# Kernel tuning notes

Hardware: AMD Instinct MI355X
Metric: run time of the kernel (lower is better)

The kernel has to match this reference:

```python
import jax, jax.numpy as jnp
import numpy as np

N_ENT = 200000  # entities per graph (sr and tg)
E = 4_000_000   # triples per graph
R_SR, R_TG, D = 1000, 1200, 128


def _cosine_sim_nbyn(a, b):
    a = a * jax.lax.rsqrt(jnp.sum(a * a, -1, keepdims=True) + 1e-8)
    b = b * jax.lax.rsqrt(jnp.sum(b * b, -1, keepdims=True) + 1e-8)
    return a @ b.T


def _relation_weighting(a, b):
    # pad to square, cosine similarity, max-pool rows/cols (MuGNN RelationWeighting)
    ra, rb = a.shape[0], b.shape[0]
    n = max(ra, rb)
    a_p = jnp.pad(a, ((0, n - ra), (0, 0)))
    b_p = jnp.pad(b, ((0, n - rb), (0, 0)))
    sim = _cosine_sim_nbyn(a_p, b_p)  # [n, n]
    return jnp.max(sim, axis=1)[:ra], jnp.max(sim, axis=0)[:rb]


def _normalize_adj(rows, cols, vals, n):
    # symmetric normalization D^-1/2 A D^-1/2 on COO values
    deg = jax.ops.segment_sum(vals, rows, num_segments=n)
    d_is = jnp.where(deg > 0, jax.lax.rsqrt(jnp.maximum(deg, 1e-12)), 0.0)
    return vals * d_is[rows] * d_is[cols]


def _adjacency_side(head, tail, conf, imp, pca, n):
    # g_func_template: elementwise product of the three aligned sparse matrices
    vals = conf * imp * pca
    # + unit (identity) matrix, then normalize; coords = [edges ; diagonal]
    diag = jnp.arange(n)
    rows = jnp.concatenate([head, diag])
    cols = jnp.concatenate([tail, diag])
    allv = jnp.concatenate([vals, jnp.ones((n,), vals.dtype)])
    return _normalize_adj(rows, cols, allv, n)  # [E+n] COO values


def setup_inputs() -> dict:
    key = jax.random.key(0)
    ks = jax.random.split(key, 14)
    return {
        "rel_emb_sr": jax.random.normal(ks[0], (R_SR, D), jnp.float32),
        "rel_emb_tg": jax.random.normal(ks[1], (R_TG, D), jnp.float32),
        "conf_sr": jax.random.uniform(ks[2], (E,), jnp.float32),
        "imp_sr": jax.random.uniform(ks[3], (E,), jnp.float32),
        "pca_sr": jax.random.uniform(ks[4], (E,), jnp.float32),
        "conf_tg": jax.random.uniform(ks[5], (E,), jnp.float32),
        "imp_tg": jax.random.uniform(ks[6], (E,), jnp.float32),
        "pca_tg": jax.random.uniform(ks[7], (E,), jnp.float32),
        "head_sr": jax.random.randint(ks[8], (E,), 0, N_ENT),
        "tail_sr": jax.random.randint(ks[9], (E,), 0, N_ENT),
        "relation_sr": jax.random.randint(ks[10], (E,), 0, R_SR),
        "head_tg": jax.random.randint(ks[11], (E,), 0, N_ENT),
        "tail_tg": jax.random.randint(ks[12], (E,), 0, N_ENT),
        "relation_tg": jax.random.randint(ks[13], (E,), 0, R_TG),
    }


def reference(rel_emb_sr, rel_emb_tg, conf_sr, imp_sr, pca_sr,
              conf_tg, imp_tg, pca_tg,
              head_sr, tail_sr, relation_sr, head_tg, tail_tg, relation_tg):
    # relation weighting (computed in the original forward; g_func_template
    # discards the gathered relation attention, so relation_sr/tg do not
    # affect the adjacency values)
    rw_sr, rw_tg = _relation_weighting(rel_emb_sr, rel_emb_tg)
    adj_sr = _adjacency_side(head_sr, tail_sr, conf_sr, imp_sr, pca_sr, N_ENT)
    adj_tg = _adjacency_side(head_tg, tail_tg, conf_tg, imp_tg, pca_tg, N_ENT)
    # adjacency returned as normalized COO values on constant coords
    return adj_sr, adj_tg, rw_sr, rw_tg
```

## Files before the change

### kernel.cpp

```cpp
#include <hip/hip_runtime.h>
#include <stdint.h>

#define N_ENT 200000
#define NEDGE 4000000
#define RSR 1000
#define RTG 1200
#define DIM 128

#define NBUCK 196
#define BUCKSZ 1024
#define CAP 22272
#define CHUNK 8192
#define NTA 512
#define NE4 (NEDGE / 4)
#define NBLK 489
#define PER (NEDGE + N_ENT)
#define PER4 (PER / 4)
#define ATILES 16
#define BTILES 19
#define NRW 2240

typedef float f32x4 __attribute__((ext_vector_type(4)));
typedef int   i32x4 __attribute__((ext_vector_type(4)));


__global__ void prep_kernel(const float* __restrict__ emb_sr, const float* __restrict__ emb_tg,
                            float* __restrict__ an, float* __restrict__ bn,
                            unsigned* __restrict__ gcount) {
    int blk = blockIdx.x, t = threadIdx.x;
    const float* src; float* dst; int row;
    if (blk < RSR) { src = emb_sr; dst = an; row = blk; }
    else           { src = emb_tg; dst = bn; row = blk - RSR; }
    float x = src[row * DIM + t];
    __shared__ float sh[DIM];
    sh[t] = x * x;
    __syncthreads();
    for (int off = 64; off > 0; off >>= 1) {
        if (t < off) sh[t] += sh[t + off];
        __syncthreads();
    }
    dst[row * DIM + t] = x * rsqrtf(sh[0] + 1e-8f);
    if (blk == 0)
        for (int i = t; i < 2 * NBUCK; i += DIM) gcount[i] = 0;
}


__global__ __launch_bounds__(NTA) void passA_kernel(
        const float* __restrict__ conf_sr, const float* __restrict__ imp_sr,
        const float* __restrict__ pca_sr,
        const float* __restrict__ conf_tg, const float* __restrict__ imp_tg,
        const float* __restrict__ pca_tg,
        const int* __restrict__ head_sr, const int* __restrict__ head_tg,
        float* __restrict__ out_sr, float* __restrict__ out_tg,
        unsigned* __restrict__ gcount, unsigned* __restrict__ regions) {
    __shared__ unsigned cnt[NBUCK];
    __shared__ unsigned offs[NBUCK];
    __shared__ unsigned gdst[NBUCK];
    __shared__ unsigned ssum[256];
    __shared__ unsigned wtot[4];
    __shared__ unsigned stage[CHUNK];

    const int t = threadIdx.x;
    const int side = (int)blockIdx.x >= NBLK;
    const int blk = side ? blockIdx.x - NBLK : blockIdx.x;
    const f32x4* conf4 = (const f32x4*)(side ? conf_tg : conf_sr);
    const f32x4* imp4  = (const f32x4*)(side ? imp_tg  : imp_sr);
    const f32x4* pca4  = (const f32x4*)(side ? pca_tg  : pca_sr);
    const i32x4* head4 = (const i32x4*)(side ? head_tg : head_sr);
    f32x4*       o4    = (f32x4*)(side ? out_tg : out_sr);

    for (int i = t; i < NBUCK; i += NTA) cnt[i] = 0;
    __syncthreads();

    int bkt[16];
    unsigned rec[16], rnk[16];
#pragma unroll
    for (int i = 0; i < 4; i++) {
        int q = blk * 2048 + t + i * NTA;
        if (q < NE4) {
            f32x4 cf = __builtin_nontemporal_load(conf4 + q);
            f32x4 im = __builtin_nontemporal_load(imp4 + q);
            f32x4 pc = __builtin_nontemporal_load(pca4 + q);
            i32x4 hh = head4[q];
            f32x4 v = cf * im * pc;
            o4[q] = v;
            const int hs[4] = {hh.x, hh.y, hh.z, hh.w};
            const float vs[4] = {v.x, v.y, v.z, v.w};
#pragma unroll
            for (int j = 0; j < 4; j++) {
                int h = hs[j];
                int bb = h >> 10;
                unsigned qv = (unsigned)(vs[j] * 16384.f + 0.5f);
                if (qv > 16383u) qv = 16383u;
                bkt[i * 4 + j] = bb;
                rec[i * 4 + j] = ((unsigned)h << 14) | qv;
                rnk[i * 4 + j] = atomicAdd(&cnt[bb], 1u);
            }
        } else {
#pragma unroll
            for (int j = 0; j < 4; j++) bkt[i * 4 + j] = -1;
        }
    }
    __syncthreads();

    if (t < 256) {
        int lane = t & 63, w = t >> 6;
        unsigned s = (t < NBUCK) ? cnt[t] : 0u;
#pragma unroll
        for (int d = 1; d < 64; d <<= 1) {
            unsigned u = __shfl_up(s, d);
            if (lane >= d) s += u;
        }
        if (lane == 63) wtot[w] = s;
        ssum[t] = s;
    }
    __syncthreads();
    unsigned wb0 = wtot[0];
    unsigned wb1 = wb0 + wtot[1];
    unsigned wb2 = wb1 + wtot[2];
    unsigned total = wb2 + wtot[3];
    if (t < NBUCK) {
        int w = t >> 6;
        unsigned add = (w == 0) ? 0u : (w == 1) ? wb0 : (w == 2) ? wb1 : wb2;
        unsigned ex = ssum[t] + add - cnt[t];
        offs[t] = ex;
        unsigned gb = atomicAdd(&gcount[side * NBUCK + t], cnt[t]);
        gdst[t] = (unsigned)(side * NBUCK + t) * CAP + gb - ex;
    }
    __syncthreads();

#pragma unroll
    for (int i = 0; i < 16; i++)
        if (bkt[i] >= 0) stage[offs[bkt[i]] + rnk[i]] = rec[i];
    __syncthreads();

    for (int i = t; i < (int)total; i += NTA) {
        unsigned r = stage[i];
        unsigned b = r >> 24;
        unsigned d = gdst[b] + i;
        if (d < (unsigned)(side * NBUCK + b + 1) * CAP) regions[d] = r;
    }
}


__global__ __launch_bounds__(256) void passB_kernel(const unsigned* __restrict__ regions,
                                                    const unsigned* __restrict__ gcount,
                                                    float* __restrict__ dis) {
    __shared__ float bins[BUCKSZ / 2];
    int t = threadIdx.x;
    int g = blockIdx.x;
    int sb = g >> 1;
    unsigned half = g & 1;
    for (int i = t; i < BUCKSZ / 2; i += 256) bins[i] = 0.f;
    __syncthreads();
    unsigned n = gcount[sb];
    if (n > CAP) n = CAP;
    const unsigned* rp = regions + (size_t)sb * CAP;
    for (unsigned i = t; i < n; i += 256) {
        unsigned r = rp[i];
        unsigned bin = (r >> 14) & (BUCKSZ - 1);
        if ((bin >> 9) == half)
            atomicAdd(&bins[bin & 511u], (float)(r & 16383u) * (1.f / 16384.f));
    }
    __syncthreads();
    int side = sb >= NBUCK;
    int b = side ? sb - NBUCK : sb;
    int base = b * BUCKSZ + (int)half * 512;
    float* dout = dis + (size_t)side * N_ENT;
    for (int i = t; i < 512; i += 256) {
        int e = base + i;
        if (e < N_ENT) dout[e] = rsqrtf(1.0f + bins[i]);
    }
}


__global__ void deg_init_kernel(float* __restrict__ dis) {
    int i = blockIdx.x * 256 + threadIdx.x;
    if (i < (2 * N_ENT) / 4)
        ((float4*)dis)[i] = make_float4(1.f, 1.f, 1.f, 1.f);
}

__global__ void scatter_atomic_kernel(
        const float* __restrict__ conf_sr, const float* __restrict__ imp_sr,
        const float* __restrict__ pca_sr,
        const float* __restrict__ conf_tg, const float* __restrict__ imp_tg,
        const float* __restrict__ pca_tg,
        const int* __restrict__ head_sr, const int* __restrict__ head_tg,
        float* __restrict__ out_sr, float* __restrict__ out_tg,
        float* __restrict__ deg) {
    int e = blockIdx.x * blockDim.x + threadIdx.x;
    if (e < NEDGE) {
        float v = conf_sr[e] * imp_sr[e] * pca_sr[e];
        out_sr[e] = v;
        unsafeAtomicAdd(&deg[head_sr[e]], v);
    } else if (e < 2 * NEDGE) {
        int i = e - NEDGE;
        float v = conf_tg[i] * imp_tg[i] * pca_tg[i];
        out_tg[i] = v;
        unsafeAtomicAdd(&deg[N_ENT + head_tg[i]], v);
    }
}

__global__ void rsqrt_kernel(float* __restrict__ dis) {
    int i = blockIdx.x * blockDim.x + threadIdx.x;
    if (i < 2 * N_ENT) dis[i] = rsqrtf(dis[i]);
}


__global__ __launch_bounds__(256) void finalize_kernel(
        const int* __restrict__ head_sr, const int* __restrict__ tail_sr,
        const int* __restrict__ head_tg, const int* __restrict__ tail_tg,
        const float* __restrict__ dis, float* __restrict__ out,
        const float* __restrict__ rowpart, const float* __restrict__ colpart,
        float* __restrict__ rw_sr, float* __restrict__ rw_tg) {
    int idx = blockIdx.x * blockDim.x + threadIdx.x;
    if (idx >= 2 * PER4) {
        int rid = idx - 2 * PER4;
        if (rid < 1024) {
            if (rid < RSR) {
                float m = -1e30f;
                for (int b = 0; b < BTILES; b++) m = fmaxf(m, rowpart[b * 1024 + rid]);
                rw_sr[rid] = m;
            }
        } else if (rid < NRW) {
            int j = rid - 1024;
            if (j < RTG) {
                float m = -1e30f;
                for (int a = 0; a < ATILES; a++) m = fmaxf(m, colpart[a * 1216 + j]);
                rw_tg[j] = fmaxf(m, 0.0f);
            }
        }
        return;
    }
    int side = idx >= PER4 ? 1 : 0;
    int q = side ? idx - PER4 : idx;
    const float* dg = dis + (size_t)side * N_ENT;
    f32x4* o = (f32x4*)(out + (size_t)side * PER);
    if (q < NE4) {
        const i32x4* hd = (const i32x4*)(side ? head_tg : head_sr);
        const i32x4* tl = (const i32x4*)(side ? tail_tg : tail_sr);
        i32x4 hh = hd[q];
        i32x4 tt = tl[q];
        f32x4 v = o[q];
        v.x *= dg[hh.x] * dg[tt.x];
        v.y *= dg[hh.y] * dg[tt.y];
        v.z *= dg[hh.z] * dg[tt.z];
        v.w *= dg[hh.w] * dg[tt.w];
        o[q] = v;
    } else {
        f32x4 d = ((const f32x4*)dg)[q - NE4];
        o[q] = d * d;
    }
}


__global__ __launch_bounds__(256) void pools_tiles_kernel(
        const float* __restrict__ an, const float* __restrict__ bn,
        float* __restrict__ rowpart, float* __restrict__ colpart) {
    __shared__ float sA[64][132];
    __shared__ float sB[64][133];
    __shared__ float rr[64][17];
    __shared__ float cc[64][17];
    int t = threadIdx.x;
    int atile = blockIdx.x % ATILES;
    int btile = blockIdx.x / ATILES;
    for (int idx = t; idx < 64 * 32; idx += 256) {
        int row = idx >> 5, k4 = idx & 31;
        int ga = atile * 64 + row;
        float4 va = (ga < RSR) ? ((const float4*)(an + ga * DIM))[k4]
                               : make_float4(0.f, 0.f, 0.f, 0.f);
        *(float4*)&sA[row][k4 * 4] = va;
        int gb = btile * 64 + row;
        float4 vb = (gb < RTG) ? ((const float4*)(bn + gb * DIM))[k4]
                               : make_float4(0.f, 0.f, 0.f, 0.f);
        sB[row][k4 * 4 + 0] = vb.x; sB[row][k4 * 4 + 1] = vb.y;
        sB[row][k4 * 4 + 2] = vb.z; sB[row][k4 * 4 + 3] = vb.w;
    }
    __syncthreads();
    int tx = t & 15, ty = t >> 4;
    float acc[4][4] = {};
    for (int k4 = 0; k4 < 32; k4++) {
        float4 a4[4];
#pragma unroll
        for (int r = 0; r < 4; r++) a4[r] = *(const float4*)&sA[ty * 4 + r][k4 * 4];
#pragma unroll
        for (int kk = 0; kk < 4; kk++) {
            float bv[4];
#pragma unroll
            for (int c = 0; c < 4; c++) bv[c] = sB[tx * 4 + c][k4 * 4 + kk];
            float av[4];
#pragma unroll
            for (int r = 0; r < 4; r++)
                av[r] = kk == 0 ? a4[r].x : kk == 1 ? a4[r].y : kk == 2 ? a4[r].z : a4[r].w;
#pragma unroll
            for (int r = 0; r < 4; r++)
#pragma unroll
                for (int c = 0; c < 4; c++) acc[r][c] = fmaf(av[r], bv[c], acc[r][c]);
        }
    }
    float rm[4] = {-1e30f, -1e30f, -1e30f, -1e30f};
    float cm[4] = {-1e30f, -1e30f, -1e30f, -1e30f};
#pragma unroll
    for (int r = 0; r < 4; r++)
#pragma unroll
        for (int c = 0; c < 4; c++) {
            bool jok = (btile * 64 + tx * 4 + c) < RTG;
            rm[r] = fmaxf(rm[r], jok ? acc[r][c] : -1e30f);
            cm[c] = fmaxf(cm[c], acc[r][c]);
        }
#pragma unroll
    for (int r = 0; r < 4; r++) rr[ty * 4 + r][tx] = rm[r];
#pragma unroll
    for (int c = 0; c < 4; c++) cc[tx * 4 + c][ty] = cm[c];
    __syncthreads();
    if (t < 64) {
        float m = rr[t][0];
        for (int x = 1; x < 16; x++) m = fmaxf(m, rr[t][x]);
        rowpart[btile * 1024 + atile * 64 + t] = m;
        float m2 = cc[t][0];
        for (int x = 1; x < 16; x++) m2 = fmaxf(m2, cc[t][x]);
        colpart[atile * 1216 + btile * 64 + t] = m2;
    }
}


extern "C" void kernel_launch(void* const* d_in, const int* in_sizes, int n_in,
                              void* d_out, int out_size, void* d_ws, size_t ws_size,
                              hipStream_t stream) {
    const float* rel_emb_sr = (const float*)d_in[0];
    const float* rel_emb_tg = (const float*)d_in[1];
    const float* conf_sr = (const float*)d_in[2];
    const float* imp_sr  = (const float*)d_in[3];
    const float* pca_sr  = (const float*)d_in[4];
    const float* conf_tg = (const float*)d_in[5];
    const float* imp_tg  = (const float*)d_in[6];
    const float* pca_tg  = (const float*)d_in[7];
    const int* head_sr = (const int*)d_in[8];
    const int* tail_sr = (const int*)d_in[9];
    const int* head_tg = (const int*)d_in[11];
    const int* tail_tg = (const int*)d_in[12];

    float* out = (float*)d_out;
    float* out_sr = out;
    float* out_tg = out + PER;
    float* rw_sr  = out + 2 * (size_t)PER;
    float* rw_tg  = rw_sr + RSR;

    float* ws = (float*)d_ws;
    float* an  = ws;
    float* bn  = an + RSR * DIM;
    float* dis = bn + RTG * DIM;
    unsigned* gcount  = (unsigned*)(dis + 2 * N_ENT);
    unsigned* regions = gcount + 512;
    float* rowpart = (float*)(regions + (size_t)2 * NBUCK * CAP);
    float* colpart = rowpart + BTILES * 1024;

    size_t need = ((size_t)(RSR * DIM + RTG * DIM + 2 * N_ENT + 512) +
                   (size_t)2 * NBUCK * CAP + BTILES * 1024 + ATILES * 1216) * 4;
    bool bucketed = ws_size >= need;

    hipLaunchKernelGGL(prep_kernel, dim3(RSR + RTG), dim3(DIM), 0, stream,
                       rel_emb_sr, rel_emb_tg, an, bn, gcount);

    if (bucketed) {
        hipLaunchKernelGGL(passA_kernel, dim3(2 * NBLK), dim3(NTA), 0, stream,
                           conf_sr, imp_sr, pca_sr, conf_tg, imp_tg, pca_tg,
                           head_sr, head_tg, out_sr, out_tg, gcount, regions);
        hipLaunchKernelGGL(passB_kernel, dim3(4 * NBUCK), dim3(256), 0, stream,
                           regions, gcount, dis);
    } else {
        hipLaunchKernelGGL(deg_init_kernel, dim3((2 * N_ENT / 4 + 255) / 256), dim3(256),
                           0, stream, dis);
        hipLaunchKernelGGL(scatter_atomic_kernel, dim3((2 * NEDGE + 255) / 256), dim3(256),
                           0, stream,
                           conf_sr, imp_sr, pca_sr, conf_tg, imp_tg, pca_tg,
                           head_sr, head_tg, out_sr, out_tg, dis);
        hipLaunchKernelGGL(rsqrt_kernel, dim3((2 * N_ENT + 255) / 256), dim3(256), 0, stream,
                           dis);
    }

    hipLaunchKernelGGL(pools_tiles_kernel, dim3(ATILES * BTILES), dim3(256), 0, stream,
                       an, bn, rowpart, colpart);

    hipLaunchKernelGGL(finalize_kernel, dim3((2 * PER4 + NRW + 255) / 256), dim3(256),
                       0, stream,
                       head_sr, tail_sr, head_tg, tail_tg, dis, out,
                       rowpart, colpart, rw_sr, rw_tg);
}
```

Baseline: 358.0 us.

## Fuse relation-weighting stages into bucketed degree passes to cut kernel launches

Folds the embedding normalization into the first bucketing pass as extra blocks, and the cosine-similarity tile pooling into the second (degree histogram) pass. A memset replaces the counter zeroing, so five launches become a memset plus three kernels. Independent small work can then overlap with the bandwidth-bound edge passes. The finalize kernel also handles both graphs per thread, halving its grid. The risk is heavier kernels with larger shared memory (the fused k2 holds tile buffers), which could lower occupancy for the histogram blocks.

```diff
diff --git a/kernel.cpp b/kernel.cpp
--- a/kernel.cpp
+++ b/kernel.cpp
@@ -14,6 +14,8 @@
 #define NTA 512
 #define NE4 (NEDGE / 4)
 #define NBLK 489
+#define NPREP 550
+#define NPOOLS 304
 #define PER (NEDGE + N_ENT)
 #define PER4 (PER / 4)
 #define ATILES 16
@@ -24,28 +26,9 @@
 typedef int   i32x4 __attribute__((ext_vector_type(4)));
 
 
-__global__ void prep_kernel(const float* __restrict__ emb_sr, const float* __restrict__ emb_tg,
-                            float* __restrict__ an, float* __restrict__ bn,
-                            unsigned* __restrict__ gcount) {
-    int blk = blockIdx.x, t = threadIdx.x;
-    const float* src; float* dst; int row;
-    if (blk < RSR) { src = emb_sr; dst = an; row = blk; }
-    else           { src = emb_tg; dst = bn; row = blk - RSR; }
-    float x = src[row * DIM + t];
-    __shared__ float sh[DIM];
-    sh[t] = x * x;
-    __syncthreads();
-    for (int off = 64; off > 0; off >>= 1) {
-        if (t < off) sh[t] += sh[t + off];
-        __syncthreads();
-    }
-    dst[row * DIM + t] = x * rsqrtf(sh[0] + 1e-8f);
-    if (blk == 0)
-        for (int i = t; i < 2 * NBUCK; i += DIM) gcount[i] = 0;
-}
-
-
-__global__ __launch_bounds__(NTA) void passA_kernel(
+__global__ __launch_bounds__(NTA) void k1_kernel(
+        const float* __restrict__ emb_sr, const float* __restrict__ emb_tg,
+        float* __restrict__ an, float* __restrict__ bn,
         const float* __restrict__ conf_sr, const float* __restrict__ imp_sr,
         const float* __restrict__ pca_sr,
         const float* __restrict__ conf_tg, const float* __restrict__ imp_tg,
@@ -53,6 +36,26 @@
         const int* __restrict__ head_sr, const int* __restrict__ head_tg,
         float* __restrict__ out_sr, float* __restrict__ out_tg,
         unsigned* __restrict__ gcount, unsigned* __restrict__ regions) {
+    const int t = threadIdx.x;
+
+    if (blockIdx.x < NPREP) {
+        __shared__ float sh[NTA];
+        int row = (int)blockIdx.x * 4 + (t >> 7);
+        int col = t & 127;
+        const float* src; float* dst;
+        if (row < RSR) { src = emb_sr + row * DIM; dst = an + row * DIM; }
+        else           { src = emb_tg + (row - RSR) * DIM; dst = bn + (row - RSR) * DIM; }
+        float x = src[col];
+        sh[t] = x * x;
+        __syncthreads();
+        for (int off = 64; off > 0; off >>= 1) {
+            if ((t & 127) < off) sh[t] += sh[t + off];
+            __syncthreads();
+        }
+        dst[col] = x * rsqrtf(sh[(t >> 7) << 7] + 1e-8f);
+        return;
+    }
+
     __shared__ unsigned cnt[NBUCK];
     __shared__ unsigned offs[NBUCK];
     __shared__ unsigned gdst[NBUCK];
@@ -60,9 +63,9 @@
     __shared__ unsigned wtot[4];
     __shared__ unsigned stage[CHUNK];
 
-    const int t = threadIdx.x;
-    const int side = (int)blockIdx.x >= NBLK;
-    const int blk = side ? blockIdx.x - NBLK : blockIdx.x;
+    const int abid = (int)blockIdx.x - NPREP;
+    const int side = abid >= NBLK;
+    const int blk = side ? abid - NBLK : abid;
     const f32x4* conf4 = (const f32x4*)(side ? conf_tg : conf_sr);
     const f32x4* imp4  = (const f32x4*)(side ? imp_tg  : imp_sr);
     const f32x4* pca4  = (const f32x4*)(side ? pca_tg  : pca_sr);
@@ -143,12 +146,87 @@
 }
 
 
-__global__ __launch_bounds__(256) void passB_kernel(const unsigned* __restrict__ regions,
-                                                    const unsigned* __restrict__ gcount,
-                                                    float* __restrict__ dis) {
+__global__ __launch_bounds__(256) void k2_kernel(
+        const float* __restrict__ an, const float* __restrict__ bn,
+        float* __restrict__ rowpart, float* __restrict__ colpart,
+        const unsigned* __restrict__ regions, const unsigned* __restrict__ gcount,
+        float* __restrict__ dis) {
+    const int t = threadIdx.x;
+
+    if (blockIdx.x < NPOOLS) {
+        __shared__ float sA[64][68];
+        __shared__ float sB[64][69];
+        __shared__ float rr[64][17];
+        __shared__ float cc[64][17];
+        int atile = (int)blockIdx.x % ATILES;
+        int btile = (int)blockIdx.x / ATILES;
+        int tx = t & 15, ty = t >> 4;
+        float acc[4][4] = {};
+        for (int kh = 0; kh < 2; kh++) {
+            for (int idx = t; idx < 64 * 16; idx += 256) {
+                int row = idx >> 4, k4 = idx & 15;
+                int ga = atile * 64 + row;
+                float4 va = (ga < RSR) ? ((const float4*)(an + ga * DIM + kh * 64))[k4]
+                                       : make_float4(0.f, 0.f, 0.f, 0.f);
+                *(float4*)&sA[row][k4 * 4] = va;
+                int gb = btile * 64 + row;
+                float4 vb = (gb < RTG) ? ((const float4*)(bn + gb * DIM + kh * 64))[k4]
+                                       : make_float4(0.f, 0.f, 0.f, 0.f);
+                sB[row][k4 * 4 + 0] = vb.x; sB[row][k4 * 4 + 1] = vb.y;
+                sB[row][k4 * 4 + 2] = vb.z; sB[row][k4 * 4 + 3] = vb.w;
+            }
+            __syncthreads();
+            for (int k4 = 0; k4 < 16; k4++) {
+                float4 a4[4];
+#pragma unroll
+                for (int r = 0; r < 4; r++) a4[r] = *(const float4*)&sA[ty * 4 + r][k4 * 4];
+#pragma unroll
+                for (int kk = 0; kk < 4; kk++) {
+                    float bv[4];
+#pragma unroll
+                    for (int c = 0; c < 4; c++) bv[c] = sB[tx * 4 + c][k4 * 4 + kk];
+                    float av[4];
+#pragma unroll
+                    for (int r = 0; r < 4; r++)
+                        av[r] = kk == 0 ? a4[r].x : kk == 1 ? a4[r].y
+                              : kk == 2 ? a4[r].z : a4[r].w;
+#pragma unroll
+                    for (int r = 0; r < 4; r++)
+#pragma unroll
+                        for (int c = 0; c < 4; c++)
+                            acc[r][c] = fmaf(av[r], bv[c], acc[r][c]);
+                }
+            }
+            __syncthreads();
+        }
+        float rm[4] = {-1e30f, -1e30f, -1e30f, -1e30f};
+        float cm[4] = {-1e30f, -1e30f, -1e30f, -1e30f};
+#pragma unroll
+        for (int r = 0; r < 4; r++)
+#pragma unroll
+            for (int c = 0; c < 4; c++) {
+                bool jok = (btile * 64 + tx * 4 + c) < RTG;
+                rm[r] = fmaxf(rm[r], jok ? acc[r][c] : -1e30f);
+                cm[c] = fmaxf(cm[c], acc[r][c]);
+            }
+#pragma unroll
+        for (int r = 0; r < 4; r++) rr[ty * 4 + r][tx] = rm[r];
+#pragma unroll
+        for (int c = 0; c < 4; c++) cc[tx * 4 + c][ty] = cm[c];
+        __syncthreads();
+        if (t < 64) {
+            float m = rr[t][0];
+            for (int x = 1; x < 16; x++) m = fmaxf(m, rr[t][x]);
+            rowpart[btile * 1024 + atile * 64 + t] = m;
+            float m2 = cc[t][0];
+            for (int x = 1; x < 16; x++) m2 = fmaxf(m2, cc[t][x]);
+            colpart[atile * 1216 + btile * 64 + t] = m2;
+        }
+        return;
+    }
+
     __shared__ float bins[BUCKSZ / 2];
-    int t = threadIdx.x;
-    int g = blockIdx.x;
+    int g = (int)blockIdx.x - NPOOLS;
     int sb = g >> 1;
     unsigned half = g & 1;
     for (int i = t; i < BUCKSZ / 2; i += 256) bins[i] = 0.f;
@@ -173,6 +251,23 @@
     }
 }
 
+
+__global__ void prep_kernel(const float* __restrict__ emb_sr, const float* __restrict__ emb_tg,
+                            float* __restrict__ an, float* __restrict__ bn) {
+    int blk = blockIdx.x, t = threadIdx.x;
+    const float* src; float* dst; int row;
+    if (blk < RSR) { src = emb_sr; dst = an; row = blk; }
+    else           { src = emb_tg; dst = bn; row = blk - RSR; }
+    float x = src[row * DIM + t];
+    __shared__ float sh[DIM];
+    sh[t] = x * x;
+    __syncthreads();
+    for (int off = 64; off > 0; off >>= 1) {
+        if (t < off) sh[t] += sh[t + off];
+        __syncthreads();
+    }
+    dst[row * DIM + t] = x * rsqrtf(sh[0] + 1e-8f);
+}
 
 __global__ void deg_init_kernel(float* __restrict__ dis) {
     int i = blockIdx.x * 256 + threadIdx.x;
@@ -205,54 +300,6 @@
     int i = blockIdx.x * blockDim.x + threadIdx.x;
     if (i < 2 * N_ENT) dis[i] = rsqrtf(dis[i]);
 }
-
-
-__global__ __launch_bounds__(256) void finalize_kernel(
-        const int* __restrict__ head_sr, const int* __restrict__ tail_sr,
-        const int* __restrict__ head_tg, const int* __restrict__ tail_tg,
-        const float* __restrict__ dis, float* __restrict__ out,
-        const float* __restrict__ rowpart, const float* __restrict__ colpart,
-        float* __restrict__ rw_sr, float* __restrict__ rw_tg) {
-    int idx = blockIdx.x * blockDim.x + threadIdx.x;
-    if (idx >= 2 * PER4) {
-        int rid = idx - 2 * PER4;
-        if (rid < 1024) {
-            if (rid < RSR) {
-                float m = -1e30f;
-                for (int b = 0; b < BTILES; b++) m = fmaxf(m, rowpart[b * 1024 + rid]);
-                rw_sr[rid] = m;
-            }
-        } else if (rid < NRW) {
-            int j = rid - 1024;
-            if (j < RTG) {
-                float m = -1e30f;
-                for (int a = 0; a < ATILES; a++) m = fmaxf(m, colpart[a * 1216 + j]);
-                rw_tg[j] = fmaxf(m, 0.0f);
-            }
-        }
-        return;
-    }
-    int side = idx >= PER4 ? 1 : 0;
-    int q = side ? idx - PER4 : idx;
-    const float* dg = dis + (size_t)side * N_ENT;
-    f32x4* o = (f32x4*)(out + (size_t)side * PER);
-    if (q < NE4) {
-        const i32x4* hd = (const i32x4*)(side ? head_tg : head_sr);
-        const i32x4* tl = (const i32x4*)(side ? tail_tg : tail_sr);
-        i32x4 hh = hd[q];
-        i32x4 tt = tl[q];
-        f32x4 v = o[q];
-        v.x *= dg[hh.x] * dg[tt.x];
-        v.y *= dg[hh.y] * dg[tt.y];
-        v.z *= dg[hh.z] * dg[tt.z];
-        v.w *= dg[hh.w] * dg[tt.w];
-        o[q] = v;
-    } else {
-        f32x4 d = ((const f32x4*)dg)[q - NE4];
-        o[q] = d * d;
-    }
-}
-
 
 __global__ __launch_bounds__(256) void pools_tiles_kernel(
         const float* __restrict__ an, const float* __restrict__ bn,
@@ -324,6 +371,59 @@
 }
 
 
+__global__ __launch_bounds__(256) void finalize_kernel(
+        const int* __restrict__ head_sr, const int* __restrict__ tail_sr,
+        const int* __restrict__ head_tg, const int* __restrict__ tail_tg,
+        const float* __restrict__ dis, float* __restrict__ out,
+        const float* __restrict__ rowpart, const float* __restrict__ colpart,
+        float* __restrict__ rw_sr, float* __restrict__ rw_tg) {
+    int idx = blockIdx.x * blockDim.x + threadIdx.x;
+    if (idx >= PER4) {
+        int rid = idx - PER4;
+        if (rid < 1024) {
+            if (rid < RSR) {
+                float m = -1e30f;
+                for (int b = 0; b < BTILES; b++) m = fmaxf(m, rowpart[b * 1024 + rid]);
+                rw_sr[rid] = m;
+            }
+        } else if (rid < NRW) {
+            int j = rid - 1024;
+            if (j < RTG) {
+                float m = -1e30f;
+                for (int a = 0; a < ATILES; a++) m = fmaxf(m, colpart[a * 1216 + j]);
+                rw_tg[j] = fmaxf(m, 0.0f);
+            }
+        }
+        return;
+    }
+    const float* dg0 = dis;
+    const float* dg1 = dis + N_ENT;
+    f32x4* o0 = (f32x4*)out;
+    f32x4* o1 = (f32x4*)(out + (size_t)PER);
+    if (idx < NE4) {
+        i32x4 h0 = ((const i32x4*)head_sr)[idx];
+        i32x4 t0 = ((const i32x4*)tail_sr)[idx];
+        i32x4 h1 = ((const i32x4*)head_tg)[idx];
+        i32x4 t1 = ((const i32x4*)tail_tg)[idx];
+        f32x4 v0 = o0[idx];
+        f32x4 v1 = o1[idx];
+        float a0 = dg0[h0.x], a1 = dg0[h0.y], a2 = dg0[h0.z], a3 = dg0[h0.w];
+        float b0 = dg0[t0.x], b1 = dg0[t0.y], b2 = dg0[t0.z], b3 = dg0[t0.w];
+        float c0 = dg1[h1.x], c1 = dg1[h1.y], c2 = dg1[h1.z], c3 = dg1[h1.w];
+        float d0 = dg1[t1.x], d1 = dg1[t1.y], d2 = dg1[t1.z], d3 = dg1[t1.w];
+        v0.x *= a0 * b0; v0.y *= a1 * b1; v0.z *= a2 * b2; v0.w *= a3 * b3;
+        v1.x *= c0 * d0; v1.y *= c1 * d1; v1.z *= c2 * d2; v1.w *= c3 * d3;
+        o0[idx] = v0;
+        o1[idx] = v1;
+    } else {
+        f32x4 e0 = ((const f32x4*)dg0)[idx - NE4];
+        f32x4 e1 = ((const f32x4*)dg1)[idx - NE4];
+        o0[idx] = e0 * e0;
+        o1[idx] = e1 * e1;
+    }
+}
+
+
 extern "C" void kernel_launch(void* const* d_in, const int* in_sizes, int n_in,
                               void* d_out, int out_size, void* d_ws, size_t ws_size,
                               hipStream_t stream) {
@@ -359,16 +459,17 @@
                    (size_t)2 * NBUCK * CAP + BTILES * 1024 + ATILES * 1216) * 4;
     bool bucketed = ws_size >= need;
 
-    hipLaunchKernelGGL(prep_kernel, dim3(RSR + RTG), dim3(DIM), 0, stream,
-                       rel_emb_sr, rel_emb_tg, an, bn, gcount);
-
     if (bucketed) {
-        hipLaunchKernelGGL(passA_kernel, dim3(2 * NBLK), dim3(NTA), 0, stream,
+        hipMemsetAsync(gcount, 0, 512 * sizeof(unsigned), stream);
+        hipLaunchKernelGGL(k1_kernel, dim3(NPREP + 2 * NBLK), dim3(NTA), 0, stream,
+                           rel_emb_sr, rel_emb_tg, an, bn,
                            conf_sr, imp_sr, pca_sr, conf_tg, imp_tg, pca_tg,
                            head_sr, head_tg, out_sr, out_tg, gcount, regions);
-        hipLaunchKernelGGL(passB_kernel, dim3(4 * NBUCK), dim3(256), 0, stream,
-                           regions, gcount, dis);
+        hipLaunchKernelGGL(k2_kernel, dim3(NPOOLS + 4 * NBUCK), dim3(256), 0, stream,
+                           an, bn, rowpart, colpart, regions, gcount, dis);
     } else {
+        hipLaunchKernelGGL(prep_kernel, dim3(RSR + RTG), dim3(DIM), 0, stream,
+                           rel_emb_sr, rel_emb_tg, an, bn);
         hipLaunchKernelGGL(deg_init_kernel, dim3((2 * N_ENT / 4 + 255) / 256), dim3(256),
                            0, stream, dis);
         hipLaunchKernelGGL(scatter_atomic_kernel, dim3((2 * NEDGE + 255) / 256), dim3(256),
@@ -377,12 +478,11 @@
                            head_sr, head_tg, out_sr, out_tg, dis);
         hipLaunchKernelGGL(rsqrt_kernel, dim3((2 * N_ENT + 255) / 256), dim3(256), 0, stream,
                            dis);
-    }
-
-    hipLaunchKernelGGL(pools_tiles_kernel, dim3(ATILES * BTILES), dim3(256), 0, stream,
-                       an, bn, rowpart, colpart);
-
-    hipLaunchKernelGGL(finalize_kernel, dim3((2 * PER4 + NRW + 255) / 256), dim3(256),
+        hipLaunchKernelGGL(pools_tiles_kernel, dim3(ATILES * BTILES), dim3(256), 0, stream,
+                           an, bn, rowpart, colpart);
+    }
+
+    hipLaunchKernelGGL(finalize_kernel, dim3((PER4 + NRW + 255) / 256), dim3(256),
                        0, stream,
                        head_sr, tail_sr, head_tg, tail_tg, dis, out,
                        rowpart, colpart, rw_sr, rw_tg);
```

New measurement: 351.9 us. Within noise of the previous version (-1.7%).
